# Kernel optimization log

Measured on AMD Instinct MI355X. Metric: run time of the kernel, lower is better.

The kernel has to match this reference:

```python
import jax, jax.numpy as jnp
import numpy as np

D_MODEL = 1024
NHEAD = 16
DFF = 4096
B = 4
L = 1024
EPS = 1e-5


def _layernorm(x, g, b):
    mu = jnp.mean(x, axis=-1, keepdims=True)
    var = jnp.mean((x - mu) ** 2, axis=-1, keepdims=True)
    return (x - mu) * jax.lax.rsqrt(var + EPS) * g + b


def _mha(q, k, v, wq, bq, wk, bk, wv, bv, wo, bo, mask=None):
    # q: [B,Lq,D], k/v: [B,Lk,D]; weights stored as [D_in, D_out]
    Bq, Lq, D = q.shape
    depth = D // NHEAD

    def split(x):  # [B,L,D] -> [B,H,L,depth]
        return x.reshape(Bq, -1, NHEAD, depth).transpose(0, 2, 1, 3)

    Q = split(q @ wq + bq)
    K = split(k @ wk + bk)
    V = split(v @ wv + bv)
    logits = jnp.einsum('bhqd,bhkd->bhqk', Q, K) / (depth ** 0.5)
    if mask is not None:
        logits = jnp.where(mask, logits, jnp.asarray(-1e9, logits.dtype))
    w = jax.nn.softmax(logits, axis=-1)
    o = jnp.einsum('bhqk,bhkd->bhqd', w, V)
    o = o.transpose(0, 2, 1, 3).reshape(Bq, -1, D)
    return o @ wo + bo


def setup_inputs() -> dict:
    key = jax.random.key(0)
    ks = jax.random.split(key, 16)
    s = 0.02

    def w(k, shp):
        return jax.random.normal(k, shp, jnp.float32) * s

    d, f = D_MODEL, DFF
    inp = {
        'tgt': jax.random.normal(ks[0], (B, L, d), jnp.float32),
        'memory': jax.random.normal(ks[1], (B, L, d), jnp.float32),
        'tgt_mask': jnp.tril(jnp.ones((L, L), jnp.bool_)),
        # self-attention params
        'sa_wq': w(ks[2], (d, d)), 'sa_bq': jnp.zeros((d,), jnp.float32),
        'sa_wk': w(ks[3], (d, d)), 'sa_bk': jnp.zeros((d,), jnp.float32),
        'sa_wv': w(ks[4], (d, d)), 'sa_bv': jnp.zeros((d,), jnp.float32),
        'sa_wo': w(ks[5], (d, d)), 'sa_bo': jnp.zeros((d,), jnp.float32),
        # cross-attention params
        'ca_wq': w(ks[6], (d, d)), 'ca_bq': jnp.zeros((d,), jnp.float32),
        'ca_wk': w(ks[7], (d, d)), 'ca_bk': jnp.zeros((d,), jnp.float32),
        'ca_wv': w(ks[8], (d, d)), 'ca_bv': jnp.zeros((d,), jnp.float32),
        'ca_wo': w(ks[9], (d, d)), 'ca_bo': jnp.zeros((d,), jnp.float32),
        # FFN params
        'ffn_w1': w(ks[10], (d, f)), 'ffn_b1': jnp.zeros((f,), jnp.float32),
        'ffn_w2': w(ks[11], (f, d)), 'ffn_b2': jnp.zeros((d,), jnp.float32),
        # LayerNorm params
        'ln1_g': jnp.ones((d,), jnp.float32), 'ln1_b': jnp.zeros((d,), jnp.float32),
        'ln2_g': jnp.ones((d,), jnp.float32), 'ln2_b': jnp.zeros((d,), jnp.float32),
        'ln3_g': jnp.ones((d,), jnp.float32), 'ln3_b': jnp.zeros((d,), jnp.float32),
    }
    return inp


def reference(tgt, memory, tgt_mask,
              sa_wq, sa_bq, sa_wk, sa_bk, sa_wv, sa_bv, sa_wo, sa_bo,
              ca_wq, ca_bq, ca_wk, ca_bk, ca_wv, ca_bv, ca_wo, ca_bo,
              ffn_w1, ffn_b1, ffn_w2, ffn_b2,
              ln1_g, ln1_b, ln2_g, ln2_b, ln3_g, ln3_b):
    # merge_mask with key_padding_mask=None -> mask used directly, broadcast over B,H
    mask = tgt_mask[None, None, :, :]
    t2 = _mha(tgt, tgt, tgt, sa_wq, sa_bq, sa_wk, sa_bk, sa_wv, sa_bv, sa_wo, sa_bo, mask)
    x = _layernorm(tgt + t2, ln1_g, ln1_b)
    t2 = _mha(x, memory, memory, ca_wq, ca_bq, ca_wk, ca_bk, ca_wv, ca_bv, ca_wo, ca_bo, None)
    x = _layernorm(x + t2, ln2_g, ln2_b)
    t2 = jax.nn.relu(x @ ffn_w1 + ffn_b1) @ ffn_w2 + ffn_b2
    x = _layernorm(x + t2, ln3_g, ln3_b)
    return x
```

## Files before the change

kernel.cpp:

```cpp
#include <hip/hip_runtime.h>
#include <hip/hip_bf16.h>

typedef unsigned short u16;
typedef __attribute__((ext_vector_type(8))) short bf16x8;
typedef __attribute__((ext_vector_type(4))) float floatx4;

__device__ inline float u2f(unsigned u) { union { unsigned i; float f; } x; x.i = u; return x.f; }
__device__ inline float bflo(unsigned p) { return u2f(p << 16); }
__device__ inline float bfhi(unsigned p) { return u2f(p & 0xffff0000u); }
__device__ inline u16 f2bf(float f) {
    union { __hip_bfloat16 h; u16 u; } x;
    x.h = __float2bfloat16(f);
    return x.u;
}
__device__ inline unsigned pk2bf(float lo, float hi) {
    return ((unsigned)f2bf(hi) << 16) | f2bf(lo);
}

#define GLDS(g, l) __builtin_amdgcn_global_load_lds( \
    (const __attribute__((address_space(1))) void*)(g), \
    (__attribute__((address_space(3))) void*)(l), 16, 0, 0)

template<int EPI, int NF>
__global__ __launch_bounds__(256, 2) void gemm_mfma(
        const u16* __restrict__ A, const u16* __restrict__ Bt,
        const float* __restrict__ bias, const u16* __restrict__ res,
        void* __restrict__ Cv, u16* __restrict__ o1, u16* __restrict__ o2,
        int N, int K)
{
    constexpr int BN = NF * 32;
    constexpr int BLOADS = BN / 64;

    __shared__ u16 As0[128 * 32];
    __shared__ u16 Bs0[BN * 32];
    __shared__ u16 As1[128 * 32];
    __shared__ u16 Bs1[BN * 32];
    __shared__ u16 As2[128 * 32];
    __shared__ u16 Bs2[BN * 32];

    const int tid = threadIdx.x;
    const int lane = tid & 63, wv = tid >> 6;
    const int wr = wv >> 1, wc = wv & 1;

    const int gx = gridDim.x;
    const int nwg = gx * gridDim.y;
    const int bid0 = blockIdx.y * gx + blockIdx.x;
    const int nbid = (bid0 & 7) * (nwg >> 3) + (bid0 >> 3);
    const int bx = nbid % gx, by = nbid / gx;
    const int row0 = by * 128, col0 = bx * BN;

    const u16* pa[2];
    int ldst[2];
    #pragma unroll
    for (int i = 0; i < 2; ++i) {
        const int idx = i * 256 + tid;
        const int r = idx >> 2;
        const int kob = (idx & 3) << 4;
        const int sw = kob ^ (((r >> 1) & 3) << 4);
        pa[i] = A + (size_t)(row0 + r) * K + (sw >> 1);
        ldst[i] = idx * 8;
    }
    const u16* pb[BLOADS];
    int ldstB[BLOADS];
    #pragma unroll
    for (int i = 0; i < BLOADS; ++i) {
        const int idx = i * 256 + tid;
        const int r = idx >> 2;
        const int kob = (idx & 3) << 4;
        const int sw = kob ^ (((r >> 1) & 3) << 4);
        pb[i] = Bt + (size_t)(col0 + r) * K + (sw >> 1);
        ldstB[i] = idx * 8;
    }

    int offa[4], offb[NF];
    const int rsel = lane & 15, slot = lane >> 4;
    #pragma unroll
    for (int m = 0; m < 4; ++m) {
        const int ra = wr * 64 + m * 16 + rsel;
        offa[m] = ra * 32 + (((slot << 4) ^ (((ra >> 1) & 3) << 4)) >> 1);
    }
    #pragma unroll
    for (int n = 0; n < NF; ++n) {
        const int rb = wc * (NF * 16) + n * 16 + rsel;
        offb[n] = rb * 32 + (((slot << 4) ^ (((rb >> 1) & 3) << 4)) >> 1);
    }

    floatx4 acc[4][NF] = {};

#define STAGE(AA, BB, t) do {                                   \
        const int ko_ = (t) << 5;                               \
        GLDS(pa[0] + ko_, &AA[ldst[0]]);                        \
        GLDS(pa[1] + ko_, &AA[ldst[1]]);                        \
        _Pragma("unroll")                                       \
        for (int i = 0; i < BLOADS; ++i)                        \
            GLDS(pb[i] + ko_, &BB[ldstB[i]]);                   \
    } while (0)

#define COMPUTE(AA, BB) do {                                    \
        bf16x8 af[4], bfr[NF];                                  \
        _Pragma("unroll")                                       \
        for (int m = 0; m < 4; ++m) af[m] = *(const bf16x8*)&AA[offa[m]]; \
        _Pragma("unroll")                                       \
        for (int n = 0; n < NF; ++n) bfr[n] = *(const bf16x8*)&BB[offb[n]]; \
        _Pragma("unroll")                                       \
        for (int m = 0; m < 4; ++m)                             \
            _Pragma("unroll")                                   \
            for (int n = 0; n < NF; ++n)                        \
                acc[m][n] = __builtin_amdgcn_mfma_f32_16x16x32_bf16( \
                        af[m], bfr[n], acc[m][n], 0, 0, 0);     \
    } while (0)

#define PHASE(CA, CB, NA, NB, t) do {                           \
        if ((t) < nkt - 1) {                                    \
            if constexpr (NF == 4)                              \
                asm volatile("s_waitcnt vmcnt(4)" ::: "memory");\
            else                                                \
                asm volatile("s_waitcnt vmcnt(3)" ::: "memory");\
        } else {                                                \
            asm volatile("s_waitcnt vmcnt(0)" ::: "memory");    \
        }                                                       \
        __builtin_amdgcn_s_barrier();                           \
        __builtin_amdgcn_sched_barrier(0);                      \
        if ((t) + 2 < nkt) STAGE(NA, NB, (t) + 2);              \
        COMPUTE(CA, CB);                                        \
    } while (0)

    const int nkt = K >> 5;
    STAGE(As0, Bs0, 0);
    STAGE(As1, Bs1, 1);
    int t = 0;
    for (; t + 3 <= nkt; t += 3) {
        PHASE(As0, Bs0, As2, Bs2, t);
        PHASE(As1, Bs1, As0, Bs0, t + 1);
        PHASE(As2, Bs2, As1, Bs1, t + 2);
    }
    if (t < nkt)     PHASE(As0, Bs0, As2, Bs2, t);
    if (t + 1 < nkt) PHASE(As1, Bs1, As0, Bs0, t + 1);
#undef STAGE
#undef COMPUTE
#undef PHASE

    const int cr4 = (lane >> 4) * 4;
    const int cc = lane & 15;

    if (EPI == 5 || EPI == 6) {
        const int seg = col0 >> 10;
        const int vtseg = (EPI == 5) ? 2 : 1;
        u16* dst;
        if (EPI == 5) dst = (seg == 0) ? (u16*)Cv : (seg == 1 ? o1 : o2);
        else          dst = (seg == 0) ? (u16*)Cv : o1;

        if (seg == vtseg) {
            #pragma unroll
            for (int n = 0; n < NF; ++n) {
                const int col = col0 + wc * (NF * 16) + n * 16 + cc;
                const float bv = bias[col];
                const int vcol = col & 1023;
                const int h = vcol >> 6, d = vcol & 63;
                #pragma unroll
                for (int m = 0; m < 4; ++m) {
                    const int tk = row0 + wr * 64 + m * 16 + cr4;
                    const int b = tk >> 10;
                    ushort4 o4;
                    o4.x = f2bf(acc[m][n][0] + bv);
                    o4.y = f2bf(acc[m][n][1] + bv);
                    o4.z = f2bf(acc[m][n][2] + bv);
                    o4.w = f2bf(acc[m][n][3] + bv);
                    *(ushort4*)(dst +
                        (((size_t)(b * 16 + h) * 64 + d) * 1024 + (tk & 1023))) = o4;
                }
            }
        } else {
            #pragma unroll
            for (int n = 0; n < NF; ++n) {
                const int col = col0 + wc * (NF * 16) + n * 16 + cc;
                const float bv = bias[col];
                const int oc = col & 1023;
                #pragma unroll
                for (int m = 0; m < 4; ++m) {
                    const int rowb = row0 + wr * 64 + m * 16 + cr4;
                    #pragma unroll
                    for (int r = 0; r < 4; ++r)
                        dst[(size_t)(rowb + r) * 1024 + oc] = f2bf(acc[m][n][r] + bv);
                }
            }
        }
        return;
    }

    #pragma unroll
    for (int n = 0; n < NF; ++n) {
        const int col = col0 + wc * (NF * 16) + n * 16 + cc;
        const float bv = bias[col];
        #pragma unroll
        for (int m = 0; m < 4; ++m) {
            const int rowb = row0 + wr * 64 + m * 16 + cr4;
            #pragma unroll
            for (int r = 0; r < 4; ++r) {
                float v = acc[m][n][r] + bv;
                const size_t o = (size_t)(rowb + r) * N + col;
                if (EPI == 2 || EPI == 3) v += u2f((unsigned)res[o] << 16);
                if (EPI == 1) v = fmaxf(v, 0.f);
                if (EPI == 3) ((float*)Cv)[o] = v;
                else          ((u16*)Cv)[o] = f2bf(v);
            }
        }
    }
}

struct TrwB { const float* w[8]; u16* o[8]; };

__global__ __launch_bounds__(256) void trw8_kernel(TrwB p)
{
    __shared__ float ts[64][65];
    const int tid = threadIdx.x;
    const int n0 = blockIdx.x * 64, k0 = blockIdx.y * 64;
    const float* __restrict__ W = p.w[blockIdx.z];
    u16* __restrict__ Wt = p.o[blockIdx.z];
    const int tr = tid >> 4, tc4 = (tid & 15) * 4;
    #pragma unroll
    for (int i = 0; i < 4; ++i) {
        const float4 v = *(const float4*)(W + (size_t)(k0 + tr + i * 16) * 1024 + n0 + tc4);
        ts[tr + i * 16][tc4 + 0] = v.x;
        ts[tr + i * 16][tc4 + 1] = v.y;
        ts[tr + i * 16][tc4 + 2] = v.z;
        ts[tr + i * 16][tc4 + 3] = v.w;
    }
    __syncthreads();
    #pragma unroll
    for (int i = 0; i < 4; ++i) {
        const int nr = tr + i * 16;
        ushort4 o;
        o.x = f2bf(ts[tc4 + 0][nr]);
        o.y = f2bf(ts[tc4 + 1][nr]);
        o.z = f2bf(ts[tc4 + 2][nr]);
        o.w = f2bf(ts[tc4 + 3][nr]);
        *(ushort4*)(Wt + (size_t)(n0 + nr) * 1024 + k0 + tc4) = o;
    }
}

__global__ __launch_bounds__(256) void trw_kernel(
        const float* __restrict__ W, u16* __restrict__ Wt, int K, int N)
{
    __shared__ float ts[64][65];
    const int tid = threadIdx.x;
    const int n0 = blockIdx.x * 64, k0 = blockIdx.y * 64;
    const int tr = tid >> 4, tc4 = (tid & 15) * 4;
    #pragma unroll
    for (int i = 0; i < 4; ++i) {
        const float4 v = *(const float4*)(W + (size_t)(k0 + tr + i * 16) * N + n0 + tc4);
        ts[tr + i * 16][tc4 + 0] = v.x;
        ts[tr + i * 16][tc4 + 1] = v.y;
        ts[tr + i * 16][tc4 + 2] = v.z;
        ts[tr + i * 16][tc4 + 3] = v.w;
    }
    __syncthreads();
    #pragma unroll
    for (int i = 0; i < 4; ++i) {
        const int nr = tr + i * 16;
        ushort4 o;
        o.x = f2bf(ts[tc4 + 0][nr]);
        o.y = f2bf(ts[tc4 + 1][nr]);
        o.z = f2bf(ts[tc4 + 2][nr]);
        o.w = f2bf(ts[tc4 + 3][nr]);
        *(ushort4*)(Wt + (size_t)(n0 + nr) * K + k0 + tc4) = o;
    }
}

__global__ __launch_bounds__(256) void cvt_kernel(
        const float* __restrict__ in, u16* __restrict__ out, int n4)
{
    for (int i = blockIdx.x * 256 + threadIdx.x; i < n4; i += gridDim.x * 256) {
        const float4 v = ((const float4*)in)[i];
        ushort4 o;
        o.x = f2bf(v.x); o.y = f2bf(v.y); o.z = f2bf(v.z); o.w = f2bf(v.w);
        ((ushort4*)out)[i] = o;
    }
}

__global__ __launch_bounds__(256) void bcat_kernel(
        const float* __restrict__ b0, const float* __restrict__ b1,
        const float* __restrict__ b2, float* __restrict__ o, int n)
{
    const int i = blockIdx.x * 256 + threadIdx.x;
    if (i >= n) return;
    const float* s = (i < 1024) ? b0 : (i < 2048 ? b1 : b2);
    o[i] = s[i & 1023];
}

template<int CAUSAL>
__global__ __launch_bounds__(256) void fattn_mfma(
        const u16* __restrict__ Q, const u16* __restrict__ K,
        const u16* __restrict__ Vt, u16* __restrict__ O)
{
    __shared__ u16 Ks[64 * 64];
    __shared__ u16 Vs[64 * 64];
    __shared__ u16 Ps[64 * 64];

    const int tid = threadIdx.x;
    const int lane = tid & 63, wv = tid >> 6;
    const int g = lane >> 4, qx = lane & 15;
    const int bh = blockIdx.x;
    const int b = bh >> 4, h = bh & 15;
    const int qt = blockIdx.y, q0 = qt * 64;
    const float SCL = 0.18033688011f;

    const size_t qkbase = (size_t)b * (1024 * 1024) + (size_t)h * 64;
    const size_t vtbase = (size_t)bh * 64 * 1024;

    const int qr = wv * 16 + qx;
    const int qg = q0 + qr;
    const int swzq = (qr & 7) << 4;

    bf16x8 qf[2];
    #pragma unroll
    for (int ks = 0; ks < 2; ++ks)
        qf[ks] = *(const bf16x8*)(Q + qkbase + (size_t)qg * 1024 + ks * 32 + g * 8);

    const int r0 = tid >> 3, s0 = tid & 7;

    float m_i = -1e30f, l_i = 0.f;
    floatx4 o_acc[4] = {};

    const int ktmax = CAUSAL ? qt : 15;
    for (int kt = 0; kt <= ktmax; ++kt) {
        __syncthreads();
        #pragma unroll
        for (int i = 0; i < 2; ++i) {
            const int r = i * 32 + r0;
            const uint4 kv = *(const uint4*)(K + qkbase + (size_t)(kt * 64 + r) * 1024 + s0 * 8);
            *(uint4*)((char*)Ks + r * 128 + ((s0 ^ (r & 7)) << 4)) = kv;
            const uint4 vv = *(const uint4*)(Vt + vtbase + (size_t)r * 1024 + kt * 64 + s0 * 8);
            *(uint4*)((char*)Vs + r * 128 + ((s0 ^ (r & 7)) << 4)) = vv;
        }
        __syncthreads();

        floatx4 sa[4] = {};
        #pragma unroll
        for (int ks = 0; ks < 2; ++ks) {
            #pragma unroll
            for (int m = 0; m < 4; ++m) {
                const int rr = m * 16 + qx;
                const int sl = ks * 4 + g;
                const bf16x8 kf = *(const bf16x8*)((char*)Ks + rr * 128 + ((sl ^ (rr & 7)) << 4));
                sa[m] = __builtin_amdgcn_mfma_f32_16x16x32_bf16(kf, qf[ks], sa[m], 0, 0, 0);
            }
        }

        float p[4][4];
        float mx = -1e30f;
        #pragma unroll
        for (int m = 0; m < 4; ++m)
            #pragma unroll
            for (int r = 0; r < 4; ++r) {
                float v = sa[m][r] * SCL;
                if (CAUSAL && kt == qt) {
                    const int kl = m * 16 + g * 4 + r;
                    if (kl > qr) v = -1e30f;
                }
                p[m][r] = v;
                mx = fmaxf(mx, v);
            }
        mx = fmaxf(mx, __shfl_xor(mx, 16));
        mx = fmaxf(mx, __shfl_xor(mx, 32));

        const float mn = fmaxf(m_i, mx);
        const float al = exp2f(m_i - mn);
        m_i = mn;
        float rs = 0.f;
        #pragma unroll
        for (int m = 0; m < 4; ++m)
            #pragma unroll
            for (int r = 0; r < 4; ++r) { p[m][r] = exp2f(p[m][r] - mn); rs += p[m][r]; }
        rs += __shfl_xor(rs, 16);
        rs += __shfl_xor(rs, 32);
        l_i = l_i * al + rs;
        #pragma unroll
        for (int n = 0; n < 4; ++n) o_acc[n] *= al;

        #pragma unroll
        for (int m = 0; m < 4; ++m) {
            uint2 pk;
            pk.x = pk2bf(p[m][0], p[m][1]);
            pk.y = pk2bf(p[m][2], p[m][3]);
            *(uint2*)((char*)Ps + qr * 128 + ((m * 32 + g * 8) ^ swzq)) = pk;
        }

        #pragma unroll
        for (int ks2 = 0; ks2 < 2; ++ks2) {
            const bf16x8 pf = *(const bf16x8*)((char*)Ps + qr * 128 + ((ks2 * 64 + g * 16) ^ swzq));
            #pragma unroll
            for (int n = 0; n < 4; ++n) {
                const int rv = n * 16 + qx;
                const int sl = ks2 * 4 + g;
                const bf16x8 vf = *(const bf16x8*)((char*)Vs + rv * 128 + ((sl ^ (rv & 7)) << 4));
                o_acc[n] = __builtin_amdgcn_mfma_f32_16x16x32_bf16(vf, pf, o_acc[n], 0, 0, 0);
            }
        }
    }

    const float inv = 1.f / l_i;
    #pragma unroll
    for (int n = 0; n < 4; ++n) {
        uint2 ov;
        ov.x = pk2bf(o_acc[n][0] * inv, o_acc[n][1] * inv);
        ov.y = pk2bf(o_acc[n][2] * inv, o_acc[n][3] * inv);
        *(uint2*)((char*)Ps + qr * 128 + ((n * 32 + g * 8) ^ swzq)) = ov;
    }
    const int orow = wv * 16 + (lane >> 2);
    const int swzo = (orow & 7) << 4;
    #pragma unroll
    for (int i = 0; i < 2; ++i) {
        const int cb = ((lane & 3) * 2 + i) * 16;
        const uint4 ov = *(const uint4*)((char*)Ps + orow * 128 + (cb ^ swzo));
        *(uint4*)(O + qkbase + (size_t)(q0 + orow) * 1024 + cb / 2) = ov;
    }
}

__global__ __launch_bounds__(256) void ln_bf16_kernel(
        const u16* __restrict__ X, const float* __restrict__ g,
        const float* __restrict__ bta, u16* __restrict__ Y)
{
    __shared__ float red[4];
    const int row = blockIdx.x, tid = threadIdx.x;
    const int wave = tid >> 6, lane = tid & 63;

    const uint2 u = *(const uint2*)(X + (size_t)row * 1024 + tid * 4);
    const float x0 = bflo(u.x), x1 = bfhi(u.x), x2 = bflo(u.y), x3 = bfhi(u.y);

    float s = x0 + x1 + x2 + x3;
    #pragma unroll
    for (int off = 32; off; off >>= 1) s += __shfl_xor(s, off);
    if (lane == 0) red[wave] = s;
    __syncthreads();
    const float mu = (red[0] + red[1] + red[2] + red[3]) * (1.f / 1024.f);
    __syncthreads();

    const float d0 = x0 - mu, d1 = x1 - mu, d2 = x2 - mu, d3 = x3 - mu;
    float s2 = d0 * d0 + d1 * d1 + d2 * d2 + d3 * d3;
    #pragma unroll
    for (int off = 32; off; off >>= 1) s2 += __shfl_xor(s2, off);
    if (lane == 0) red[wave] = s2;
    __syncthreads();
    const float var = (red[0] + red[1] + red[2] + red[3]) * (1.f / 1024.f);
    const float rs = rsqrtf(var + 1e-5f);

    const float4 gg = ((const float4*)g)[tid];
    const float4 bb = ((const float4*)bta)[tid];
    ushort4 o;
    o.x = f2bf(d0 * rs * gg.x + bb.x);
    o.y = f2bf(d1 * rs * gg.y + bb.y);
    o.z = f2bf(d2 * rs * gg.z + bb.z);
    o.w = f2bf(d3 * rs * gg.w + bb.w);
    *(ushort4*)(Y + (size_t)row * 1024 + tid * 4) = o;
}

__global__ __launch_bounds__(256) void ln_kernel(
        const float* X, const float* __restrict__ g,
        const float* __restrict__ bta, float* Y)
{
    __shared__ float red[4];
    const int row = blockIdx.x;
    const int tid = threadIdx.x;
    const int wave = tid >> 6, lane = tid & 63;

    const float4 v = ((const float4*)(X + (size_t)row * 1024))[tid];

    float s = v.x + v.y + v.z + v.w;
    #pragma unroll
    for (int off = 32; off; off >>= 1) s += __shfl_xor(s, off);
    if (lane == 0) red[wave] = s;
    __syncthreads();
    const float mu = (red[0] + red[1] + red[2] + red[3]) * (1.f / 1024.f);
    __syncthreads();

    const float dx = v.x - mu, dy = v.y - mu, dz = v.z - mu, dw = v.w - mu;
    float s2 = dx * dx + dy * dy + dz * dz + dw * dw;
    #pragma unroll
    for (int off = 32; off; off >>= 1) s2 += __shfl_xor(s2, off);
    if (lane == 0) red[wave] = s2;
    __syncthreads();
    const float var = (red[0] + red[1] + red[2] + red[3]) * (1.f / 1024.f);
    const float rs = rsqrtf(var + 1e-5f);

    const float4 gg = ((const float4*)g)[tid];
    const float4 bb = ((const float4*)bta)[tid];
    float4 o;
    o.x = dx * rs * gg.x + bb.x;
    o.y = dy * rs * gg.y + bb.y;
    o.z = dz * rs * gg.z + bb.z;
    o.w = dw * rs * gg.w + bb.w;
    ((float4*)(Y + (size_t)row * 1024))[tid] = o;
}

extern "C" void kernel_launch(void* const* d_in, const int* in_sizes, int n_in,
                              void* d_out, int out_size, void* d_ws, size_t ws_size,
                              hipStream_t stream)
{
    const float* tgt    = (const float*)d_in[0];
    const float* mem    = (const float*)d_in[1];
    const float* sa_wq  = (const float*)d_in[3];
    const float* sa_bq  = (const float*)d_in[4];
    const float* sa_wk  = (const float*)d_in[5];
    const float* sa_bk  = (const float*)d_in[6];
    const float* sa_wv  = (const float*)d_in[7];
    const float* sa_bv  = (const float*)d_in[8];
    const float* sa_wo  = (const float*)d_in[9];
    const float* sa_bo  = (const float*)d_in[10];
    const float* ca_wq  = (const float*)d_in[11];
    const float* ca_bq  = (const float*)d_in[12];
    const float* ca_wk  = (const float*)d_in[13];
    const float* ca_bk  = (const float*)d_in[14];
    const float* ca_wv  = (const float*)d_in[15];
    const float* ca_bv  = (const float*)d_in[16];
    const float* ca_wo  = (const float*)d_in[17];
    const float* ca_bo  = (const float*)d_in[18];
    const float* ffn_w1 = (const float*)d_in[19];
    const float* ffn_b1 = (const float*)d_in[20];
    const float* ffn_w2 = (const float*)d_in[21];
    const float* ffn_b2 = (const float*)d_in[22];
    const float* ln1_g  = (const float*)d_in[23];
    const float* ln1_b  = (const float*)d_in[24];
    const float* ln2_g  = (const float*)d_in[25];
    const float* ln2_b  = (const float*)d_in[26];
    const float* ln3_g  = (const float*)d_in[27];
    const float* ln3_b  = (const float*)d_in[28];

    float* out = (float*)d_out;
    u16* wsb = (u16*)d_ws;
    const size_t M1 = 1024 * 1024;

    u16* Wsq = wsb + 0 * M1;
    u16* Wsk = wsb + 1 * M1;
    u16* Wsv = wsb + 2 * M1;
    u16* Wso = wsb + 3 * M1;
    u16* Wcq = wsb + 4 * M1;
    u16* Wck = wsb + 5 * M1;
    u16* Wcv = wsb + 6 * M1;
    u16* Wco = wsb + 7 * M1;
    u16* Wf1 = wsb + 8 * M1;
    u16* Wf2 = wsb + 12 * M1;

    u16* sl = wsb + 16 * M1;
    u16* s0 = sl + 0 * 4 * M1;
    u16* s1 = sl + 4 * M1;
    u16* s2 = sl + 8 * M1;
    u16* s3 = sl + 12 * M1;
    u16* s4 = sl + 16 * M1;
    u16* s5 = sl + 20 * M1;
    u16* H  = s0;

    float* biasQKV = (float*)(wsb + 40 * M1);
    float* biasKV  = biasQKV + 3072;

    const dim3 blk(256);
    const dim3 gqkv(24, 32);
    const dim3 gkv(16, 32);
    const dim3 g1(16, 32);
    const dim3 g4(32, 32);
    const dim3 ga(64, 16);
    const dim3 gln(4096);

    TrwB tb;
    tb.w[0] = sa_wq; tb.o[0] = Wsq;
    tb.w[1] = sa_wk; tb.o[1] = Wsk;
    tb.w[2] = sa_wv; tb.o[2] = Wsv;
    tb.w[3] = sa_wo; tb.o[3] = Wso;
    tb.w[4] = ca_wq; tb.o[4] = Wcq;
    tb.w[5] = ca_wk; tb.o[5] = Wck;
    tb.w[6] = ca_wv; tb.o[6] = Wcv;
    tb.w[7] = ca_wo; tb.o[7] = Wco;
    trw8_kernel<<<dim3(16, 16, 8), blk, 0, stream>>>(tb);
    trw_kernel<<<dim3(64, 16), blk, 0, stream>>>(ffn_w1, Wf1, 1024, 4096);
    trw_kernel<<<dim3(16, 64), blk, 0, stream>>>(ffn_w2, Wf2, 4096, 1024);
    bcat_kernel<<<12, blk, 0, stream>>>(sa_bq, sa_bk, sa_bv, biasQKV, 3072);
    bcat_kernel<<<8, blk, 0, stream>>>(ca_bk, ca_bv, ca_bv, biasKV, 2048);
    cvt_kernel<<<2048, blk, 0, stream>>>(tgt, s0, 1024 * 1024);
    cvt_kernel<<<2048, blk, 0, stream>>>(mem, s1, 1024 * 1024);

    gemm_mfma<5, 4><<<gqkv, blk, 0, stream>>>(s0, Wsq, biasQKV, nullptr,
                                              s2, s3, s4, 3072, 1024);
    fattn_mfma<1><<<ga, blk, 0, stream>>>(s2, s3, s4, s5);
    gemm_mfma<2, 2><<<g1, blk, 0, stream>>>(s5, Wso, sa_bo, s0, s2, nullptr, nullptr, 1024, 1024);
    ln_bf16_kernel<<<gln, blk, 0, stream>>>(s2, ln1_g, ln1_b, s3);

    gemm_mfma<0, 2><<<g1, blk, 0, stream>>>(s3, Wcq, ca_bq, nullptr, s2, nullptr, nullptr, 1024, 1024);
    gemm_mfma<6, 4><<<gkv, blk, 0, stream>>>(s1, Wck, biasKV, nullptr,
                                             s4, s5, nullptr, 2048, 1024);
    fattn_mfma<0><<<ga, blk, 0, stream>>>(s2, s4, s5, s0);
    gemm_mfma<2, 2><<<g1, blk, 0, stream>>>(s0, Wco, ca_bo, s3, s2, nullptr, nullptr, 1024, 1024);
    ln_bf16_kernel<<<gln, blk, 0, stream>>>(s2, ln2_g, ln2_b, s4);

    gemm_mfma<1, 4><<<g4, blk, 0, stream>>>(s4, Wf1, ffn_b1, nullptr, H, nullptr, nullptr, 4096, 1024);
    gemm_mfma<3, 2><<<g1, blk, 0, stream>>>(H, Wf2, ffn_b2, s4, out, nullptr, nullptr, 1024, 4096);
    ln_kernel<<<gln, blk, 0, stream>>>(out, ln3_g, ln3_b, out);
}
```

Baseline: 348.5 us.

## Split-K FFN2 with atomics, 128-row attention tiles, residual folded into final LN

```diff
diff --git a/kernel.cpp b/kernel.cpp
--- a/kernel.cpp
+++ b/kernel.cpp
@@ -49,6 +49,9 @@
     const int bx = nbid % gx, by = nbid / gx;
     const int row0 = by * 128, col0 = bx * BN;
 
+    const int Keff = (EPI == 7) ? (K >> 1) : K;
+    const int k0off = (EPI == 7) ? blockIdx.z * Keff : 0;
+
     const u16* pa[2];
     int ldst[2];
     #pragma unroll
@@ -57,7 +60,7 @@
         const int r = idx >> 2;
         const int kob = (idx & 3) << 4;
         const int sw = kob ^ (((r >> 1) & 3) << 4);
-        pa[i] = A + (size_t)(row0 + r) * K + (sw >> 1);
+        pa[i] = A + (size_t)(row0 + r) * K + k0off + (sw >> 1);
         ldst[i] = idx * 8;
     }
     const u16* pb[BLOADS];
@@ -68,7 +71,7 @@
         const int r = idx >> 2;
         const int kob = (idx & 3) << 4;
         const int sw = kob ^ (((r >> 1) & 3) << 4);
-        pb[i] = Bt + (size_t)(col0 + r) * K + (sw >> 1);
+        pb[i] = Bt + (size_t)(col0 + r) * K + k0off + (sw >> 1);
         ldstB[i] = idx * 8;
     }
 
@@ -125,7 +128,7 @@
         COMPUTE(CA, CB);                                        \
     } while (0)
 
-    const int nkt = K >> 5;
+    const int nkt = Keff >> 5;
     STAGE(As0, Bs0, 0);
     STAGE(As1, Bs1, 1);
     int t = 0;
@@ -142,6 +145,24 @@
 
     const int cr4 = (lane >> 4) * 4;
     const int cc = lane & 15;
+
+    if (EPI == 7) {
+        float* outf = (float*)Cv;
+        const bool addb = (blockIdx.z == 0);
+        #pragma unroll
+        for (int n = 0; n < NF; ++n) {
+            const int col = col0 + wc * (NF * 16) + n * 16 + cc;
+            const float bv = addb ? bias[col] : 0.f;
+            #pragma unroll
+            for (int m = 0; m < 4; ++m) {
+                const int rowb = row0 + wr * 64 + m * 16 + cr4;
+                #pragma unroll
+                for (int r = 0; r < 4; ++r)
+                    atomicAdd(&outf[(size_t)(rowb + r) * N + col], acc[m][n][r] + bv);
+            }
+        }
+        return;
+    }
 
     if (EPI == 5 || EPI == 6) {
         const int seg = col0 >> 10;
@@ -199,10 +220,9 @@
             for (int r = 0; r < 4; ++r) {
                 float v = acc[m][n][r] + bv;
                 const size_t o = (size_t)(rowb + r) * N + col;
-                if (EPI == 2 || EPI == 3) v += u2f((unsigned)res[o] << 16);
+                if (EPI == 2) v += u2f((unsigned)res[o] << 16);
                 if (EPI == 1) v = fmaxf(v, 0.f);
-                if (EPI == 3) ((float*)Cv)[o] = v;
-                else          ((u16*)Cv)[o] = f2bf(v);
+                ((u16*)Cv)[o] = f2bf(v);
             }
         }
     }
@@ -278,6 +298,13 @@
     }
 }
 
+__global__ __launch_bounds__(256) void zero_kernel(float* __restrict__ p, int n4)
+{
+    const float4 z = {0.f, 0.f, 0.f, 0.f};
+    for (int i = blockIdx.x * 256 + threadIdx.x; i < n4; i += gridDim.x * 256)
+        ((float4*)p)[i] = z;
+}
+
 __global__ __launch_bounds__(256) void bcat_kernel(
         const float* __restrict__ b0, const float* __restrict__ b1,
         const float* __restrict__ b2, float* __restrict__ o, int n)
@@ -295,34 +322,38 @@
 {
     __shared__ u16 Ks[64 * 64];
     __shared__ u16 Vs[64 * 64];
-    __shared__ u16 Ps[64 * 64];
+    __shared__ u16 Ps[128 * 64];
 
     const int tid = threadIdx.x;
     const int lane = tid & 63, wv = tid >> 6;
     const int g = lane >> 4, qx = lane & 15;
     const int bh = blockIdx.x;
     const int b = bh >> 4, h = bh & 15;
-    const int qt = blockIdx.y, q0 = qt * 64;
+    const int qt = blockIdx.y, q0 = qt * 128;
     const float SCL = 0.18033688011f;
 
     const size_t qkbase = (size_t)b * (1024 * 1024) + (size_t)h * 64;
     const size_t vtbase = (size_t)bh * 64 * 1024;
 
-    const int qr = wv * 16 + qx;
-    const int qg = q0 + qr;
-    const int swzq = (qr & 7) << 4;
-
-    bf16x8 qf[2];
-    #pragma unroll
-    for (int ks = 0; ks < 2; ++ks)
-        qf[ks] = *(const bf16x8*)(Q + qkbase + (size_t)qg * 1024 + ks * 32 + g * 8);
+    int qr[2], swzq[2];
+    bf16x8 qf[2][2];
+    #pragma unroll
+    for (int f = 0; f < 2; ++f) {
+        qr[f] = wv * 32 + f * 16 + qx;
+        swzq[f] = (qr[f] & 7) << 4;
+        const int qg = q0 + qr[f];
+        #pragma unroll
+        for (int ks = 0; ks < 2; ++ks)
+            qf[f][ks] = *(const bf16x8*)(Q + qkbase + (size_t)qg * 1024 + ks * 32 + g * 8);
+    }
 
     const int r0 = tid >> 3, s0 = tid & 7;
 
-    float m_i = -1e30f, l_i = 0.f;
-    floatx4 o_acc[4] = {};
-
-    const int ktmax = CAUSAL ? qt : 15;
+    float m_i[2] = {-1e30f, -1e30f};
+    float l_i[2] = {0.f, 0.f};
+    floatx4 o_acc[2][4] = {};
+
+    const int ktmax = CAUSAL ? (2 * qt + 1) : 15;
     for (int kt = 0; kt <= ktmax; ++kt) {
         __syncthreads();
         #pragma unroll
@@ -335,83 +366,101 @@
         }
         __syncthreads();
 
-        floatx4 sa[4] = {};
-        #pragma unroll
-        for (int ks = 0; ks < 2; ++ks) {
+        bf16x8 kf[2][4];
+        #pragma unroll
+        for (int ks = 0; ks < 2; ++ks)
             #pragma unroll
             for (int m = 0; m < 4; ++m) {
-                const int rr = m * 16 + qx;
-                const int sl = ks * 4 + g;
-                const bf16x8 kf = *(const bf16x8*)((char*)Ks + rr * 128 + ((sl ^ (rr & 7)) << 4));
-                sa[m] = __builtin_amdgcn_mfma_f32_16x16x32_bf16(kf, qf[ks], sa[m], 0, 0, 0);
+                const int rr = m * 16 + qx, sl = ks * 4 + g;
+                kf[ks][m] = *(const bf16x8*)((char*)Ks + rr * 128 + ((sl ^ (rr & 7)) << 4));
+            }
+
+        #pragma unroll
+        for (int f = 0; f < 2; ++f) {
+            floatx4 sa[4] = {};
+            #pragma unroll
+            for (int ks = 0; ks < 2; ++ks)
+                #pragma unroll
+                for (int m = 0; m < 4; ++m)
+                    sa[m] = __builtin_amdgcn_mfma_f32_16x16x32_bf16(
+                            kf[ks][m], qf[f][ks], sa[m], 0, 0, 0);
+
+            float p[4][4];
+            float mx = -1e30f;
+            #pragma unroll
+            for (int m = 0; m < 4; ++m)
+                #pragma unroll
+                for (int r = 0; r < 4; ++r) {
+                    float v = sa[m][r] * SCL;
+                    if (CAUSAL && kt >= 2 * qt) {
+                        const int kl = kt * 64 + m * 16 + g * 4 + r;
+                        if (kl > q0 + qr[f]) v = -1e30f;
+                    }
+                    p[m][r] = v;
+                    mx = fmaxf(mx, v);
+                }
+            mx = fmaxf(mx, __shfl_xor(mx, 16));
+            mx = fmaxf(mx, __shfl_xor(mx, 32));
+
+            const float mn = fmaxf(m_i[f], mx);
+            const float al = exp2f(m_i[f] - mn);
+            m_i[f] = mn;
+            float rs = 0.f;
+            #pragma unroll
+            for (int m = 0; m < 4; ++m)
+                #pragma unroll
+                for (int r = 0; r < 4; ++r) { p[m][r] = exp2f(p[m][r] - mn); rs += p[m][r]; }
+            rs += __shfl_xor(rs, 16);
+            rs += __shfl_xor(rs, 32);
+            l_i[f] = l_i[f] * al + rs;
+            #pragma unroll
+            for (int n = 0; n < 4; ++n) o_acc[f][n] *= al;
+
+            #pragma unroll
+            for (int m = 0; m < 4; ++m) {
+                uint2 pk;
+                pk.x = pk2bf(p[m][0], p[m][1]);
+                pk.y = pk2bf(p[m][2], p[m][3]);
+                *(uint2*)((char*)Ps + qr[f] * 128 + ((m * 32 + g * 8) ^ swzq[f])) = pk;
             }
         }
 
-        float p[4][4];
-        float mx = -1e30f;
-        #pragma unroll
-        for (int m = 0; m < 4; ++m)
-            #pragma unroll
-            for (int r = 0; r < 4; ++r) {
-                float v = sa[m][r] * SCL;
-                if (CAUSAL && kt == qt) {
-                    const int kl = m * 16 + g * 4 + r;
-                    if (kl > qr) v = -1e30f;
-                }
-                p[m][r] = v;
-                mx = fmaxf(mx, v);
-            }
-        mx = fmaxf(mx, __shfl_xor(mx, 16));
-        mx = fmaxf(mx, __shfl_xor(mx, 32));
-
-        const float mn = fmaxf(m_i, mx);
-        const float al = exp2f(m_i - mn);
-        m_i = mn;
-        float rs = 0.f;
-        #pragma unroll
-        for (int m = 0; m < 4; ++m)
-            #pragma unroll
-            for (int r = 0; r < 4; ++r) { p[m][r] = exp2f(p[m][r] - mn); rs += p[m][r]; }
-        rs += __shfl_xor(rs, 16);
-        rs += __shfl_xor(rs, 32);
-        l_i = l_i * al + rs;
-        #pragma unroll
-        for (int n = 0; n < 4; ++n) o_acc[n] *= al;
-
-        #pragma unroll
-        for (int m = 0; m < 4; ++m) {
-            uint2 pk;
-            pk.x = pk2bf(p[m][0], p[m][1]);
-            pk.y = pk2bf(p[m][2], p[m][3]);
-            *(uint2*)((char*)Ps + qr * 128 + ((m * 32 + g * 8) ^ swzq)) = pk;
+        #pragma unroll
+        for (int ks2 = 0; ks2 < 2; ++ks2) {
+            bf16x8 vf[4];
+            #pragma unroll
+            for (int n = 0; n < 4; ++n) {
+                const int rv = n * 16 + qx, sl = ks2 * 4 + g;
+                vf[n] = *(const bf16x8*)((char*)Vs + rv * 128 + ((sl ^ (rv & 7)) << 4));
+            }
+            #pragma unroll
+            for (int f = 0; f < 2; ++f) {
+                const bf16x8 pf = *(const bf16x8*)((char*)Ps + qr[f] * 128 +
+                                                   ((ks2 * 64 + g * 16) ^ swzq[f]));
+                #pragma unroll
+                for (int n = 0; n < 4; ++n)
+                    o_acc[f][n] = __builtin_amdgcn_mfma_f32_16x16x32_bf16(
+                            vf[n], pf, o_acc[f][n], 0, 0, 0);
+            }
         }
-
-        #pragma unroll
-        for (int ks2 = 0; ks2 < 2; ++ks2) {
-            const bf16x8 pf = *(const bf16x8*)((char*)Ps + qr * 128 + ((ks2 * 64 + g * 16) ^ swzq));
-            #pragma unroll
-            for (int n = 0; n < 4; ++n) {
-                const int rv = n * 16 + qx;
-                const int sl = ks2 * 4 + g;
-                const bf16x8 vf = *(const bf16x8*)((char*)Vs + rv * 128 + ((sl ^ (rv & 7)) << 4));
-                o_acc[n] = __builtin_amdgcn_mfma_f32_16x16x32_bf16(vf, pf, o_acc[n], 0, 0, 0);
-            }
+    }
+
+    #pragma unroll
+    for (int f = 0; f < 2; ++f) {
+        const float inv = 1.f / l_i[f];
+        #pragma unroll
+        for (int n = 0; n < 4; ++n) {
+            uint2 ov;
+            ov.x = pk2bf(o_acc[f][n][0] * inv, o_acc[f][n][1] * inv);
+            ov.y = pk2bf(o_acc[f][n][2] * inv, o_acc[f][n][3] * inv);
+            *(uint2*)((char*)Ps + qr[f] * 128 + ((n * 32 + g * 8) ^ swzq[f])) = ov;
         }
     }
-
-    const float inv = 1.f / l_i;
-    #pragma unroll
-    for (int n = 0; n < 4; ++n) {
-        uint2 ov;
-        ov.x = pk2bf(o_acc[n][0] * inv, o_acc[n][1] * inv);
-        ov.y = pk2bf(o_acc[n][2] * inv, o_acc[n][3] * inv);
-        *(uint2*)((char*)Ps + qr * 128 + ((n * 32 + g * 8) ^ swzq)) = ov;
-    }
-    const int orow = wv * 16 + (lane >> 2);
+    const int orow = wv * 32 + (lane >> 1);
     const int swzo = (orow & 7) << 4;
     #pragma unroll
-    for (int i = 0; i < 2; ++i) {
-        const int cb = ((lane & 3) * 2 + i) * 16;
+    for (int i = 0; i < 4; ++i) {
+        const int cb = ((lane & 1) * 4 + i) * 16;
         const uint4 ov = *(const uint4*)((char*)Ps + orow * 128 + (cb ^ swzo));
         *(uint4*)(O + qkbase + (size_t)(q0 + orow) * 1024 + cb / 2) = ov;
     }
@@ -455,8 +504,8 @@
     *(ushort4*)(Y + (size_t)row * 1024 + tid * 4) = o;
 }
 
-__global__ __launch_bounds__(256) void ln_kernel(
-        const float* X, const float* __restrict__ g,
+__global__ __launch_bounds__(256) void ln_res_kernel(
+        const float* X, const u16* __restrict__ res, const float* __restrict__ g,
         const float* __restrict__ bta, float* Y)
 {
     __shared__ float red[4];
@@ -465,8 +514,11 @@
     const int wave = tid >> 6, lane = tid & 63;
 
     const float4 v = ((const float4*)(X + (size_t)row * 1024))[tid];
-
-    float s = v.x + v.y + v.z + v.w;
+    const uint2 u = *(const uint2*)(res + (size_t)row * 1024 + tid * 4);
+    const float x0 = v.x + bflo(u.x), x1 = v.y + bfhi(u.x);
+    const float x2 = v.z + bflo(u.y), x3 = v.w + bfhi(u.y);
+
+    float s = x0 + x1 + x2 + x3;
     #pragma unroll
     for (int off = 32; off; off >>= 1) s += __shfl_xor(s, off);
     if (lane == 0) red[wave] = s;
@@ -474,8 +526,8 @@
     const float mu = (red[0] + red[1] + red[2] + red[3]) * (1.f / 1024.f);
     __syncthreads();
 
-    const float dx = v.x - mu, dy = v.y - mu, dz = v.z - mu, dw = v.w - mu;
-    float s2 = dx * dx + dy * dy + dz * dz + dw * dw;
+    const float d0 = x0 - mu, d1 = x1 - mu, d2 = x2 - mu, d3 = x3 - mu;
+    float s2 = d0 * d0 + d1 * d1 + d2 * d2 + d3 * d3;
     #pragma unroll
     for (int off = 32; off; off >>= 1) s2 += __shfl_xor(s2, off);
     if (lane == 0) red[wave] = s2;
@@ -486,10 +538,10 @@
     const float4 gg = ((const float4*)g)[tid];
     const float4 bb = ((const float4*)bta)[tid];
     float4 o;
-    o.x = dx * rs * gg.x + bb.x;
-    o.y = dy * rs * gg.y + bb.y;
-    o.z = dz * rs * gg.z + bb.z;
-    o.w = dw * rs * gg.w + bb.w;
+    o.x = d0 * rs * gg.x + bb.x;
+    o.y = d1 * rs * gg.y + bb.y;
+    o.z = d2 * rs * gg.z + bb.z;
+    o.w = d3 * rs * gg.w + bb.w;
     ((float4*)(Y + (size_t)row * 1024))[tid] = o;
 }
 
@@ -558,7 +610,8 @@
     const dim3 gkv(16, 32);
     const dim3 g1(16, 32);
     const dim3 g4(32, 32);
-    const dim3 ga(64, 16);
+    const dim3 gf2(8, 32, 2);
+    const dim3 ga(64, 8);
     const dim3 gln(4096);
 
     TrwB tb;
@@ -577,6 +630,7 @@
     bcat_kernel<<<8, blk, 0, stream>>>(ca_bk, ca_bv, ca_bv, biasKV, 2048);
     cvt_kernel<<<2048, blk, 0, stream>>>(tgt, s0, 1024 * 1024);
     cvt_kernel<<<2048, blk, 0, stream>>>(mem, s1, 1024 * 1024);
+    zero_kernel<<<2048, blk, 0, stream>>>(out, 1024 * 1024);
 
     gemm_mfma<5, 4><<<gqkv, blk, 0, stream>>>(s0, Wsq, biasQKV, nullptr,
                                               s2, s3, s4, 3072, 1024);
@@ -592,6 +646,6 @@
     ln_bf16_kernel<<<gln, blk, 0, stream>>>(s2, ln2_g, ln2_b, s4);
 
     gemm_mfma<1, 4><<<g4, blk, 0, stream>>>(s4, Wf1, ffn_b1, nullptr, H, nullptr, nullptr, 4096, 1024);
-    gemm_mfma<3, 2><<<g1, blk, 0, stream>>>(H, Wf2, ffn_b2, s4, out, nullptr, nullptr, 1024, 4096);
-    ln_kernel<<<gln, blk, 0, stream>>>(out, ln3_g, ln3_b, out);
-}
+    gemm_mfma<7, 4><<<gf2, blk, 0, stream>>>(H, Wf2, ffn_b2, nullptr, out, nullptr, nullptr, 1024, 4096);
+    ln_res_kernel<<<gln, blk, 0, stream>>>(out, s4, ln3_g, ln3_b, out);
+}
```

Result: slower. 375.1 us (+7.6%).
